# Kernel optimization log

Hardware: AMD Instinct MI355X
Metric: run time of the kernel (lower is better)

Reference implementation:

```python
import jax, jax.numpy as jnp
import numpy as np

TAU = 2.0
EPS = 1e-5
SG_ALPHA = 4.0  # spikingjelly default Sigmoid surrogate alpha


@jax.custom_vjp
def heaviside(x):
    return (x >= 0.0).astype(x.dtype)

def _heaviside_fwd(x):
    return heaviside(x), x

def _heaviside_bwd(x, g):
    s = jax.nn.sigmoid(SG_ALPHA * x)
    return (g * SG_ALPHA * s * (1.0 - s),)

heaviside.defvjp(_heaviside_fwd, _heaviside_bwd)


def lif(x_seq, v_th):
    """Multi-step LIF, hard reset to 0, detach_reset=True. x_seq: (T, ...)."""
    def step(v, x_t):
        v = v + (x_t - v) / TAU
        s = heaviside(v - v_th)
        v = v * (1.0 - jax.lax.stop_gradient(s))  # detached hard reset
        return v, s
    _, spikes = jax.lax.scan(step, jnp.zeros_like(x_seq[0]), x_seq)
    return spikes


def bn(y, gamma, beta, mean, var):
    # y: (T, B, C, N); inference-mode BatchNorm1d over channel dim
    inv = gamma / jnp.sqrt(var + EPS)
    return y * inv[None, None, :, None] + (beta - mean * inv)[None, None, :, None]


def setup_inputs() -> dict:
    key = jax.random.key(0)
    ks = jax.random.split(key, 8)
    T, B, C, H, W = 4, 32, 256, 32, 32
    d = {
        "x": jax.random.normal(ks[0], (T, B, C, H, W), jnp.float32),
        "q_w": jax.random.normal(ks[1], (C, C), jnp.float32) * (1.0 / np.sqrt(C)),
        "q_gamma": jnp.ones((C,), jnp.float32),
        "q_beta": jnp.zeros((C,), jnp.float32),
        "q_mean": jnp.zeros((C,), jnp.float32),
        "q_var": jnp.ones((C,), jnp.float32),
        "k_w": jax.random.normal(ks[2], (C, C), jnp.float32) * (1.0 / np.sqrt(C)),
        "k_gamma": jnp.ones((C,), jnp.float32),
        "k_beta": jnp.zeros((C,), jnp.float32),
        "k_mean": jnp.zeros((C,), jnp.float32),
        "k_var": jnp.ones((C,), jnp.float32),
        "p_w": jax.random.normal(ks[3], (C, C), jnp.float32) * (1.0 / np.sqrt(C)),
        "p_b": jnp.zeros((C,), jnp.float32),
        "p_gamma": jnp.ones((C,), jnp.float32),
        "p_beta": jnp.zeros((C,), jnp.float32),
        "p_mean": jnp.zeros((C,), jnp.float32),
        "p_var": jnp.ones((C,), jnp.float32),
    }
    return d


def reference(x, q_w, q_gamma, q_beta, q_mean, q_var,
              k_w, k_gamma, k_beta, k_mean, k_var,
              p_w, p_b, p_gamma, p_beta, p_mean, p_var):
    T, B, C, H, W = x.shape
    num_heads = 8
    dh = C // num_heads
    N = H * W
    xs = x.reshape(T, B, C, N)

    # Q branch: 1x1 conv (C x C matmul) -> BN -> LIF
    q = bn(jnp.einsum('oc,tbcn->tbon', q_w, xs), q_gamma, q_beta, q_mean, q_var)
    q_spikes = lif(q, 1.0)                                # (T,B,C,N)
    q_h = q_spikes.reshape(T, B, num_heads, dh, N)

    # K branch
    k = bn(jnp.einsum('oc,tbcn->tbon', k_w, xs), k_gamma, k_beta, k_mean, k_var)
    k_spikes = lif(k, 1.0)
    k_h = k_spikes.reshape(T, B, num_heads, dh, N)

    # channel-sum pooled Q per head -> attn LIF (v_th=0.5) -> elementwise mult with K
    q_sum = jnp.sum(q_h, axis=3, keepdims=True)           # (T,B,h,1,N)
    attn = lif(q_sum, 0.5)
    x_one = attn * k_h                                    # (T,B,h,dh,N)

    # projection: 1x1 conv with bias -> BN -> LIF
    xo = x_one.reshape(T, B, C, N)
    xo = jnp.einsum('oc,tbcn->tbon', p_w, xo) + p_b[None, None, :, None]
    xo = bn(xo, p_gamma, p_beta, p_mean, p_var).reshape(T, B, C, H, W)
    x_final = lif(xo, 1.0)
    return x_final
```

## Files before the change

kernel.cpp:

```cpp
#include <hip/hip_runtime.h>
#include <cstdint>
#include <cstddef>

#define T_DIM 4
#define B_DIM 32
#define C_DIM 256
#define N_DIM 1024
#define NHEAD 8
#define DHEAD 32
#define NWRD 32

__device__ __forceinline__ float lif_step(float& v, float x, float vth) {
    v = __fadd_rn(v, __fmul_rn(__fsub_rn(x, v), 0.5f));
    const float s = (v >= vth) ? 1.0f : 0.0f;
    if (s != 0.0f) v = 0.0f;
    return s;
}

__device__ __forceinline__ void async_copy16(const float* g, float* l) {
    __builtin_amdgcn_global_load_lds(
        (const __attribute__((address_space(1))) unsigned int*)g,
        (__attribute__((address_space(3))) unsigned int*)l, 16, 0, 0);
}

#define FMA_ROW(r, av)                                \
    acc[(r)*8+0] = fmaf(av, b0.x, acc[(r)*8+0]);      \
    acc[(r)*8+1] = fmaf(av, b0.y, acc[(r)*8+1]);      \
    acc[(r)*8+2] = fmaf(av, b0.z, acc[(r)*8+2]);      \
    acc[(r)*8+3] = fmaf(av, b0.w, acc[(r)*8+3]);      \
    acc[(r)*8+4] = fmaf(av, b1.x, acc[(r)*8+4]);      \
    acc[(r)*8+5] = fmaf(av, b1.y, acc[(r)*8+5]);      \
    acc[(r)*8+6] = fmaf(av, b1.z, acc[(r)*8+6]);      \
    acc[(r)*8+7] = fmaf(av, b1.w, acc[(r)*8+7]);

#define FMA_8x8()        \
    FMA_ROW(0, a0.x)     \
    FMA_ROW(1, a0.y)     \
    FMA_ROW(2, a0.z)     \
    FMA_ROW(3, a0.w)     \
    FMA_ROW(4, a1.x)     \
    FMA_ROW(5, a1.y)     \
    FMA_ROW(6, a1.z)     \
    FMA_ROW(7, a1.w)

__global__ __launch_bounds__(256) void k_transpose(
    const float* __restrict__ qw, const float* __restrict__ kw,
    const float* __restrict__ pw, float* __restrict__ wqk_t,
    float* __restrict__ p_t)
{
    const int i = blockIdx.x * 256 + threadIdx.x;
    if (i < C_DIM * 512) {
        const int k = i >> 9, col = i & 511;
        const int h = col >> 6, j = col & 63;
        wqk_t[i] = (j < 32) ? qw[(size_t)(h * 32 + j) * C_DIM + k]
                            : kw[(size_t)(h * 32 + j - 32) * C_DIM + k];
    } else {
        const int i2 = i - C_DIM * 512;
        const int k = i2 >> 8, c = i2 & 255;
        p_t[i2] = pw[(size_t)c * C_DIM + k];
    }
}

__global__ __launch_bounds__(256, 3) void k_qk(
    const float* __restrict__ x, const float* __restrict__ wqk,
    const float* __restrict__ qg, const float* __restrict__ qbeta,
    const float* __restrict__ qmean, const float* __restrict__ qvar,
    const float* __restrict__ kg, const float* __restrict__ kbeta,
    const float* __restrict__ kmean, const float* __restrict__ kvar,
    uint32_t* __restrict__ xbits)
{
    __shared__ float w_lds[32 * 128];
    __shared__ float x_lds[32 * 128];
    __shared__ float inv_lds[128];
    __shared__ float bias_lds[128];
    float*    qsum_lds = x_lds;
    float*    attn_lds = x_lds + 256;
    uint32_t* pack_lds = (uint32_t*)(x_lds + 512);

    const int tid = threadIdx.x;
    const int hp = blockIdx.x, nt = blockIdx.y, b = blockIdx.z;
    const int n0g = nt * 128;

    const int  mg   = tid >> 4;
    const int  m0   = mg << 3;
    const int  ng   = tid & 15;
    const int  n0   = ng << 2;
    const int  hsel = mg >> 3;
    const bool is_q = ((mg & 7) < 4);

    if (tid < 128) {
        const int m = tid;
        const int hs = m >> 6, j = m & 63;
        const int h = hp * 2 + hs;
        const bool q = (j < 32);
        const float* g  = q ? qg    : kg;
        const float* be = q ? qbeta : kbeta;
        const float* me = q ? qmean : kmean;
        const float* va = q ? qvar  : kvar;
        const int ch = h * DHEAD + (q ? j : j - 32);
        const float iv = __fdiv_rn(g[ch], __fsqrt_rn(__fadd_rn(va[ch], 1e-5f)));
        inv_lds[m]  = iv;
        bias_lds[m] = __fsub_rn(be[ch], __fmul_rn(me[ch], iv));
    }

    const int skl  = tid >> 5;
    const int scol = (tid & 31) << 2;
    const float* wgp = wqk + (size_t)skl * 512 + hp * 128 + scol;

    float vstate[64];
    #pragma unroll
    for (int i = 0; i < 64; i++) vstate[i] = 0.0f;
    float v_attn = 0.0f;

    for (int t = 0; t < T_DIM; ++t) {
        float acc[64];
        #pragma unroll
        for (int i = 0; i < 64; i++) acc[i] = 0.0f;

        const float* xgp = x + ((size_t)(t * B_DIM + b) * C_DIM + skl) * N_DIM
                           + n0g + scol;

        for (int c = 0; c < 8; ++c) {
            const int kk = c * 32;
            __syncthreads();
            #pragma unroll
            for (int r = 0; r < 4; r++) {
                async_copy16(wgp + (size_t)(kk + r * 8) * 512, w_lds + r * 1024 + tid * 4);
                async_copy16(xgp + (size_t)(kk + r * 8) * N_DIM, x_lds + r * 1024 + tid * 4);
            }
            __syncthreads();
            #pragma unroll 2
            for (int k = 0; k < 32; k++) {
                const float4 a0 = *(const float4*)(w_lds + k * 128 + m0);
                const float4 a1 = *(const float4*)(w_lds + k * 128 + m0 + 4);
                const float4 b0 = *(const float4*)(x_lds + k * 128 + n0);
                const float4 b1 = *(const float4*)(x_lds + k * 128 + 64 + n0);
                FMA_8x8()
            }
        }

        #pragma unroll
        for (int r = 0; r < 8; r++) {
            const float iv = inv_lds[m0 + r];
            const float bs = bias_lds[m0 + r];
            #pragma unroll
            for (int j = 0; j < 8; j++) {
                const float y = __fadd_rn(__fmul_rn(acc[r * 8 + j], iv), bs);
                acc[r * 8 + j] = lif_step(vstate[r * 8 + j], y, 1.0f);
            }
        }

        __syncthreads();
        qsum_lds[tid] = 0.0f;
        pack_lds[tid] = 0u;
        __syncthreads();

        if (is_q) {
            #pragma unroll
            for (int j = 0; j < 8; j++) {
                const int col = (j < 4) ? (n0 + j) : (64 + n0 + (j - 4));
                float cs = acc[j];
                #pragma unroll
                for (int r = 1; r < 8; r++) cs += acc[r * 8 + j];
                atomicAdd(&qsum_lds[hsel * 128 + col], cs);
            }
        }
        __syncthreads();
        attn_lds[tid] = lif_step(v_attn, qsum_lds[tid], 0.5f);
        __syncthreads();

        if (!is_q) {
            #pragma unroll
            for (int r = 0; r < 8; r++) {
                const int krow = ((mg & 7) - 4) * 8 + r;
                #pragma unroll
                for (int ci = 0; ci < 2; ci++) {
                    uint32_t nib = 0;
                    #pragma unroll
                    for (int jj = 0; jj < 4; jj++) {
                        const int col = ci * 64 + n0 + jj;
                        if (acc[r * 8 + ci * 4 + jj] != 0.0f &&
                            attn_lds[hsel * 128 + col] != 0.0f)
                            nib |= (1u << jj);
                    }
                    if (nib) {
                        const int word = ci * 2 + (ng >> 3);
                        const int shf  = (ng & 7) * 4;
                        atomicOr(&pack_lds[hsel * 128 + krow * 4 + word], nib << shf);
                    }
                }
            }
        }
        __syncthreads();
        {
            const int hs2  = tid >> 7;
            const int rem  = tid & 127;
            const int krow = rem >> 2, word = rem & 3;
            const int ch = (hp * 2 + hs2) * DHEAD + krow;
            xbits[((size_t)(t * B_DIM + b) * C_DIM + ch) * NWRD + nt * 4 + word]
                = pack_lds[tid];
        }
    }
}

__global__ __launch_bounds__(256, 3) void k_proj(
    const uint32_t* __restrict__ xbits, const float* __restrict__ pt,
    const float* __restrict__ pbias, const float* __restrict__ pg,
    const float* __restrict__ pbeta, const float* __restrict__ pmean,
    const float* __restrict__ pvar, float* __restrict__ out)
{
    __shared__ float w_lds[32 * 128];
    __shared__ float x_lds[32 * 128];
    __shared__ float inv_lds[128];
    __shared__ float bias_lds[128];
    __shared__ float pb_lds[128];

    const int tid = threadIdx.x;
    const int mt = blockIdx.x, nt = blockIdx.y, b = blockIdx.z;
    const int n0g = nt * 128;
    const int c0  = mt * 128;

    const int mg = tid >> 4, m0 = mg << 3;
    const int ng = tid & 15, n0 = ng << 2;

    if (tid < 128) {
        const int ch = c0 + tid;
        const float iv = __fdiv_rn(pg[ch], __fsqrt_rn(__fadd_rn(pvar[ch], 1e-5f)));
        inv_lds[tid]  = iv;
        bias_lds[tid] = __fsub_rn(pbeta[ch], __fmul_rn(pmean[ch], iv));
        pb_lds[tid]   = pbias[ch];
    }

    const int skl  = tid >> 5;
    const int scol = (tid & 31) << 2;
    const float* wgp = pt + (size_t)skl * 256 + c0 + scol;

    const int urow = tid >> 3, cg = tid & 7;
    const int wsel = nt * 4 + (cg >> 1);
    const int ushf = (cg & 1) * 16;
    float* xw = x_lds + tid * 16;

    float vstate[64];
    #pragma unroll
    for (int i = 0; i < 64; i++) vstate[i] = 0.0f;

    for (int t = 0; t < T_DIM; ++t) {
        float acc[64];
        #pragma unroll
        for (int i = 0; i < 64; i++) acc[i] = 0.0f;

        const uint32_t* xg = xbits + (size_t)(t * B_DIM + b) * C_DIM * NWRD;

        uint32_t u = xg[(size_t)urow * NWRD + wsel];

        for (int c = 0; c < 8; ++c) {
            __syncthreads();
            {
                const uint32_t bits = (u >> ushf) & 0xffffu;
                #pragma unroll
                for (int q4 = 0; q4 < 4; q4++) {
                    float4 f;
                    f.x = ((bits >> (q4 * 4 + 0)) & 1u) ? 1.0f : 0.0f;
                    f.y = ((bits >> (q4 * 4 + 1)) & 1u) ? 1.0f : 0.0f;
                    f.z = ((bits >> (q4 * 4 + 2)) & 1u) ? 1.0f : 0.0f;
                    f.w = ((bits >> (q4 * 4 + 3)) & 1u) ? 1.0f : 0.0f;
                    *(float4*)(xw + q4 * 4) = f;
                }
            }
            #pragma unroll
            for (int r = 0; r < 4; r++)
                async_copy16(wgp + (size_t)(c * 32 + r * 8) * 256,
                             w_lds + r * 1024 + tid * 4);
            __syncthreads();
            if (c + 1 < 8)
                u = xg[(size_t)((c + 1) * 32 + urow) * NWRD + wsel];
            #pragma unroll 2
            for (int k = 0; k < 32; k++) {
                const float4 a0 = *(const float4*)(w_lds + k * 128 + m0);
                const float4 a1 = *(const float4*)(w_lds + k * 128 + m0 + 4);
                const float4 b0 = *(const float4*)(x_lds + k * 128 + n0);
                const float4 b1 = *(const float4*)(x_lds + k * 128 + 64 + n0);
                FMA_8x8()
            }
        }

        #pragma unroll
        for (int r = 0; r < 8; r++) {
            const int ch = c0 + m0 + r;
            const float iv = inv_lds[m0 + r];
            const float bs = bias_lds[m0 + r];
            const float pb = pb_lds[m0 + r];
            float* ob = out + ((size_t)(t * B_DIM + b) * C_DIM + ch) * N_DIM + n0g;
            float oAv[4], oBv[4];
            #pragma unroll
            for (int j = 0; j < 8; j++) {
                float y = __fadd_rn(acc[r * 8 + j], pb);
                y = __fadd_rn(__fmul_rn(y, iv), bs);
                const float s = lif_step(vstate[r * 8 + j], y, 1.0f);
                if (j < 4) oAv[j] = s; else oBv[j - 4] = s;
            }
            float4 oA, oB;
            oA.x = oAv[0]; oA.y = oAv[1]; oA.z = oAv[2]; oA.w = oAv[3];
            oB.x = oBv[0]; oB.y = oBv[1]; oB.z = oBv[2]; oB.w = oBv[3];
            *(float4*)(ob + n0)      = oA;
            *(float4*)(ob + 64 + n0) = oB;
        }
    }
}

extern "C" void kernel_launch(void* const* d_in, const int* in_sizes, int n_in,
                              void* d_out, int out_size, void* d_ws, size_t ws_size,
                              hipStream_t stream) {
    const float* x    = (const float*)d_in[0];
    const float* q_w  = (const float*)d_in[1];
    const float* q_g  = (const float*)d_in[2];
    const float* q_b  = (const float*)d_in[3];
    const float* q_m  = (const float*)d_in[4];
    const float* q_v  = (const float*)d_in[5];
    const float* k_w  = (const float*)d_in[6];
    const float* k_g  = (const float*)d_in[7];
    const float* k_b  = (const float*)d_in[8];
    const float* k_m  = (const float*)d_in[9];
    const float* k_v  = (const float*)d_in[10];
    const float* p_w  = (const float*)d_in[11];
    const float* p_b  = (const float*)d_in[12];
    const float* p_g  = (const float*)d_in[13];
    const float* p_be = (const float*)d_in[14];
    const float* p_m  = (const float*)d_in[15];
    const float* p_v  = (const float*)d_in[16];

    float*    wqk_t = (float*)d_ws;
    float*    p_t   = (float*)((char*)d_ws + 524288);
    uint32_t* xbits = (uint32_t*)((char*)d_ws + 786432);
    float*    out   = (float*)d_out;

    k_transpose<<<768, 256, 0, stream>>>(q_w, k_w, p_w, wqk_t, p_t);

    dim3 g1(NHEAD / 2, N_DIM / 128, B_DIM);
    k_qk<<<g1, 256, 0, stream>>>(x, wqk_t, q_g, q_b, q_m, q_v,
                                 k_g, k_b, k_m, k_v, xbits);

    dim3 g2(C_DIM / 128, N_DIM / 128, B_DIM);
    k_proj<<<g2, 256, 0, stream>>>(xbits, p_t, p_b, p_g, p_be, p_m, p_v, out);
}
```

Baseline: 829.0 us.

## Double-buffer LDS tiles in qk and proj kernels, flattening time and K loops

Both GEMM kernels now keep two LDS buffers and issue async global-to-LDS copies for the next K-chunk while the current one is being multiplied. The time and K-chunk loops are merged into a single 32-step loop, so prefetching also crosses timestep boundaries, leaving one barrier per step. The goal is to hide global load latency behind FMA work. The cost is twice the LDS footprint and launch bounds lowered from 3 to 2 blocks per CU, which cuts occupancy.

```diff
diff --git a/kernel.cpp b/kernel.cpp
--- a/kernel.cpp
+++ b/kernel.cpp
@@ -61,7 +61,7 @@
     }
 }
 
-__global__ __launch_bounds__(256, 3) void k_qk(
+__global__ __launch_bounds__(256, 2) void k_qk(
     const float* __restrict__ x, const float* __restrict__ wqk,
     const float* __restrict__ qg, const float* __restrict__ qbeta,
     const float* __restrict__ qmean, const float* __restrict__ qvar,
@@ -69,13 +69,13 @@
     const float* __restrict__ kmean, const float* __restrict__ kvar,
     uint32_t* __restrict__ xbits)
 {
-    __shared__ float w_lds[32 * 128];
-    __shared__ float x_lds[32 * 128];
+    __shared__ float w_lds[2][32 * 128];
+    __shared__ float x_lds[2][32 * 128];
     __shared__ float inv_lds[128];
     __shared__ float bias_lds[128];
-    float*    qsum_lds = x_lds;
-    float*    attn_lds = x_lds + 256;
-    uint32_t* pack_lds = (uint32_t*)(x_lds + 512);
+    __shared__ float    qsum_lds[256];
+    __shared__ float    attn_lds[256];
+    __shared__ uint32_t pack_lds[256];
 
     const int tid = threadIdx.x;
     const int hp = blockIdx.x, nt = blockIdx.y, b = blockIdx.z;
@@ -112,105 +112,120 @@
     for (int i = 0; i < 64; i++) vstate[i] = 0.0f;
     float v_attn = 0.0f;
 
-    for (int t = 0; t < T_DIM; ++t) {
-        float acc[64];
+    {
+        const float* xgp = x + ((size_t)b * C_DIM + skl) * N_DIM + n0g + scol;
         #pragma unroll
-        for (int i = 0; i < 64; i++) acc[i] = 0.0f;
-
-        const float* xgp = x + ((size_t)(t * B_DIM + b) * C_DIM + skl) * N_DIM
-                           + n0g + scol;
-
-        for (int c = 0; c < 8; ++c) {
-            const int kk = c * 32;
-            __syncthreads();
+        for (int r = 0; r < 4; r++) {
+            async_copy16(wgp + (size_t)(r * 8) * 512,  &w_lds[0][r * 1024 + tid * 4]);
+            async_copy16(xgp + (size_t)(r * 8) * N_DIM, &x_lds[0][r * 1024 + tid * 4]);
+        }
+    }
+
+    float acc[64];
+    #pragma unroll
+    for (int i = 0; i < 64; i++) acc[i] = 0.0f;
+
+    for (int g = 0; g < 32; ++g) {
+        const int cur = g & 1;
+        __syncthreads();
+        if (g + 1 < 32) {
+            const int g1 = g + 1, tt = g1 >> 3, kk = (g1 & 7) * 32;
+            const float* xgp = x + ((size_t)(tt * B_DIM + b) * C_DIM + kk + skl) * N_DIM
+                               + n0g + scol;
+            float* wd = &w_lds[1 - cur][0];
+            float* xd = &x_lds[1 - cur][0];
             #pragma unroll
             for (int r = 0; r < 4; r++) {
-                async_copy16(wgp + (size_t)(kk + r * 8) * 512, w_lds + r * 1024 + tid * 4);
-                async_copy16(xgp + (size_t)(kk + r * 8) * N_DIM, x_lds + r * 1024 + tid * 4);
-            }
-            __syncthreads();
+                async_copy16(wgp + (size_t)(kk + r * 8) * 512,  wd + r * 1024 + tid * 4);
+                async_copy16(xgp + (size_t)(r * 8) * N_DIM,     xd + r * 1024 + tid * 4);
+            }
+        }
+        {
+            const float* wl = &w_lds[cur][0];
+            const float* xl = &x_lds[cur][0];
             #pragma unroll 2
             for (int k = 0; k < 32; k++) {
-                const float4 a0 = *(const float4*)(w_lds + k * 128 + m0);
-                const float4 a1 = *(const float4*)(w_lds + k * 128 + m0 + 4);
-                const float4 b0 = *(const float4*)(x_lds + k * 128 + n0);
-                const float4 b1 = *(const float4*)(x_lds + k * 128 + 64 + n0);
+                const float4 a0 = *(const float4*)(wl + k * 128 + m0);
+                const float4 a1 = *(const float4*)(wl + k * 128 + m0 + 4);
+                const float4 b0 = *(const float4*)(xl + k * 128 + n0);
+                const float4 b1 = *(const float4*)(xl + k * 128 + 64 + n0);
                 FMA_8x8()
             }
         }
 
-        #pragma unroll
-        for (int r = 0; r < 8; r++) {
-            const float iv = inv_lds[m0 + r];
-            const float bs = bias_lds[m0 + r];
-            #pragma unroll
-            for (int j = 0; j < 8; j++) {
-                const float y = __fadd_rn(__fmul_rn(acc[r * 8 + j], iv), bs);
-                acc[r * 8 + j] = lif_step(vstate[r * 8 + j], y, 1.0f);
-            }
-        }
-
-        __syncthreads();
-        qsum_lds[tid] = 0.0f;
-        pack_lds[tid] = 0u;
-        __syncthreads();
-
-        if (is_q) {
-            #pragma unroll
-            for (int j = 0; j < 8; j++) {
-                const int col = (j < 4) ? (n0 + j) : (64 + n0 + (j - 4));
-                float cs = acc[j];
+        if ((g & 7) == 7) {
+            const int t = g >> 3;
+            #pragma unroll
+            for (int r = 0; r < 8; r++) {
+                const float iv = inv_lds[m0 + r];
+                const float bs = bias_lds[m0 + r];
                 #pragma unroll
-                for (int r = 1; r < 8; r++) cs += acc[r * 8 + j];
-                atomicAdd(&qsum_lds[hsel * 128 + col], cs);
-            }
-        }
-        __syncthreads();
-        attn_lds[tid] = lif_step(v_attn, qsum_lds[tid], 0.5f);
-        __syncthreads();
-
-        if (!is_q) {
-            #pragma unroll
-            for (int r = 0; r < 8; r++) {
-                const int krow = ((mg & 7) - 4) * 8 + r;
+                for (int j = 0; j < 8; j++) {
+                    const float y = __fadd_rn(__fmul_rn(acc[r * 8 + j], iv), bs);
+                    acc[r * 8 + j] = lif_step(vstate[r * 8 + j], y, 1.0f);
+                }
+            }
+            qsum_lds[tid] = 0.0f;
+            pack_lds[tid] = 0u;
+            __syncthreads();
+            if (is_q) {
                 #pragma unroll
-                for (int ci = 0; ci < 2; ci++) {
-                    uint32_t nib = 0;
+                for (int j = 0; j < 8; j++) {
+                    const int col = (j < 4) ? (n0 + j) : (64 + n0 + (j - 4));
+                    float cs = acc[j];
                     #pragma unroll
-                    for (int jj = 0; jj < 4; jj++) {
-                        const int col = ci * 64 + n0 + jj;
-                        if (acc[r * 8 + ci * 4 + jj] != 0.0f &&
-                            attn_lds[hsel * 128 + col] != 0.0f)
-                            nib |= (1u << jj);
-                    }
-                    if (nib) {
-                        const int word = ci * 2 + (ng >> 3);
-                        const int shf  = (ng & 7) * 4;
-                        atomicOr(&pack_lds[hsel * 128 + krow * 4 + word], nib << shf);
+                    for (int r = 1; r < 8; r++) cs += acc[r * 8 + j];
+                    atomicAdd(&qsum_lds[hsel * 128 + col], cs);
+                }
+            }
+            __syncthreads();
+            attn_lds[tid] = lif_step(v_attn, qsum_lds[tid], 0.5f);
+            __syncthreads();
+            if (!is_q) {
+                #pragma unroll
+                for (int r = 0; r < 8; r++) {
+                    const int krow = ((mg & 7) - 4) * 8 + r;
+                    #pragma unroll
+                    for (int ci = 0; ci < 2; ci++) {
+                        uint32_t nib = 0;
+                        #pragma unroll
+                        for (int jj = 0; jj < 4; jj++) {
+                            const int col = ci * 64 + n0 + jj;
+                            if (acc[r * 8 + ci * 4 + jj] != 0.0f &&
+                                attn_lds[hsel * 128 + col] != 0.0f)
+                                nib |= (1u << jj);
+                        }
+                        if (nib) {
+                            const int word = ci * 2 + (ng >> 3);
+                            const int shf  = (ng & 7) * 4;
+                            atomicOr(&pack_lds[hsel * 128 + krow * 4 + word], nib << shf);
+                        }
                     }
                 }
             }
-        }
-        __syncthreads();
-        {
-            const int hs2  = tid >> 7;
-            const int rem  = tid & 127;
-            const int krow = rem >> 2, word = rem & 3;
-            const int ch = (hp * 2 + hs2) * DHEAD + krow;
-            xbits[((size_t)(t * B_DIM + b) * C_DIM + ch) * NWRD + nt * 4 + word]
-                = pack_lds[tid];
-        }
-    }
-}
-
-__global__ __launch_bounds__(256, 3) void k_proj(
+            __syncthreads();
+            {
+                const int hs2  = tid >> 7;
+                const int rem  = tid & 127;
+                const int krow = rem >> 2, word = rem & 3;
+                const int ch = (hp * 2 + hs2) * DHEAD + krow;
+                xbits[((size_t)(t * B_DIM + b) * C_DIM + ch) * NWRD + nt * 4 + word]
+                    = pack_lds[tid];
+            }
+            #pragma unroll
+            for (int i = 0; i < 64; i++) acc[i] = 0.0f;
+        }
+    }
+}
+
+__global__ __launch_bounds__(256, 2) void k_proj(
     const uint32_t* __restrict__ xbits, const float* __restrict__ pt,
     const float* __restrict__ pbias, const float* __restrict__ pg,
     const float* __restrict__ pbeta, const float* __restrict__ pmean,
     const float* __restrict__ pvar, float* __restrict__ out)
 {
-    __shared__ float w_lds[32 * 128];
-    __shared__ float x_lds[32 * 128];
+    __shared__ float w_lds[2][32 * 128];
+    __shared__ float x_lds[2][32 * 128];
     __shared__ float inv_lds[128];
     __shared__ float bias_lds[128];
     __shared__ float pb_lds[128];
@@ -238,74 +253,100 @@
     const int urow = tid >> 3, cg = tid & 7;
     const int wsel = nt * 4 + (cg >> 1);
     const int ushf = (cg & 1) * 16;
-    float* xw = x_lds + tid * 16;
 
     float vstate[64];
     #pragma unroll
     for (int i = 0; i < 64; i++) vstate[i] = 0.0f;
 
-    for (int t = 0; t < T_DIM; ++t) {
-        float acc[64];
+    #define BITS_AT(G) xbits[((size_t)((G) >> 3) * B_DIM + b) * C_DIM * NWRD \
+                             + (size_t)(((G) & 7) * 32 + urow) * NWRD + wsel]
+
+    {
+        const uint32_t u0 = BITS_AT(0);
+        const uint32_t bits = (u0 >> ushf) & 0xffffu;
+        float* xw = &x_lds[0][tid * 16];
         #pragma unroll
-        for (int i = 0; i < 64; i++) acc[i] = 0.0f;
-
-        const uint32_t* xg = xbits + (size_t)(t * B_DIM + b) * C_DIM * NWRD;
-
-        uint32_t u = xg[(size_t)urow * NWRD + wsel];
-
-        for (int c = 0; c < 8; ++c) {
-            __syncthreads();
-            {
-                const uint32_t bits = (u >> ushf) & 0xffffu;
-                #pragma unroll
-                for (int q4 = 0; q4 < 4; q4++) {
-                    float4 f;
-                    f.x = ((bits >> (q4 * 4 + 0)) & 1u) ? 1.0f : 0.0f;
-                    f.y = ((bits >> (q4 * 4 + 1)) & 1u) ? 1.0f : 0.0f;
-                    f.z = ((bits >> (q4 * 4 + 2)) & 1u) ? 1.0f : 0.0f;
-                    f.w = ((bits >> (q4 * 4 + 3)) & 1u) ? 1.0f : 0.0f;
-                    *(float4*)(xw + q4 * 4) = f;
-                }
-            }
+        for (int q4 = 0; q4 < 4; q4++) {
+            float4 f;
+            f.x = ((bits >> (q4 * 4 + 0)) & 1u) ? 1.0f : 0.0f;
+            f.y = ((bits >> (q4 * 4 + 1)) & 1u) ? 1.0f : 0.0f;
+            f.z = ((bits >> (q4 * 4 + 2)) & 1u) ? 1.0f : 0.0f;
+            f.w = ((bits >> (q4 * 4 + 3)) & 1u) ? 1.0f : 0.0f;
+            *(float4*)(xw + q4 * 4) = f;
+        }
+        #pragma unroll
+        for (int r = 0; r < 4; r++)
+            async_copy16(wgp + (size_t)(r * 8) * 256, &w_lds[0][r * 1024 + tid * 4]);
+    }
+    uint32_t u_a = BITS_AT(1);
+
+    float acc[64];
+    #pragma unroll
+    for (int i = 0; i < 64; i++) acc[i] = 0.0f;
+
+    for (int g = 0; g < 32; ++g) {
+        const int cur = g & 1;
+        __syncthreads();
+        if (g + 1 < 32) {
+            const int kk = ((g + 1) & 7) * 32;
+            const uint32_t bits = (u_a >> ushf) & 0xffffu;
+            float* xw = &x_lds[1 - cur][tid * 16];
+            #pragma unroll
+            for (int q4 = 0; q4 < 4; q4++) {
+                float4 f;
+                f.x = ((bits >> (q4 * 4 + 0)) & 1u) ? 1.0f : 0.0f;
+                f.y = ((bits >> (q4 * 4 + 1)) & 1u) ? 1.0f : 0.0f;
+                f.z = ((bits >> (q4 * 4 + 2)) & 1u) ? 1.0f : 0.0f;
+                f.w = ((bits >> (q4 * 4 + 3)) & 1u) ? 1.0f : 0.0f;
+                *(float4*)(xw + q4 * 4) = f;
+            }
+            float* wd = &w_lds[1 - cur][0];
             #pragma unroll
             for (int r = 0; r < 4; r++)
-                async_copy16(wgp + (size_t)(c * 32 + r * 8) * 256,
-                             w_lds + r * 1024 + tid * 4);
-            __syncthreads();
-            if (c + 1 < 8)
-                u = xg[(size_t)((c + 1) * 32 + urow) * NWRD + wsel];
+                async_copy16(wgp + (size_t)(kk + r * 8) * 256, wd + r * 1024 + tid * 4);
+        }
+        if (g + 2 < 32) u_a = BITS_AT(g + 2);
+        {
+            const float* wl = &w_lds[cur][0];
+            const float* xl = &x_lds[cur][0];
             #pragma unroll 2
             for (int k = 0; k < 32; k++) {
-                const float4 a0 = *(const float4*)(w_lds + k * 128 + m0);
-                const float4 a1 = *(const float4*)(w_lds + k * 128 + m0 + 4);
-                const float4 b0 = *(const float4*)(x_lds + k * 128 + n0);
-                const float4 b1 = *(const float4*)(x_lds + k * 128 + 64 + n0);
+                const float4 a0 = *(const float4*)(wl + k * 128 + m0);
+                const float4 a1 = *(const float4*)(wl + k * 128 + m0 + 4);
+                const float4 b0 = *(const float4*)(xl + k * 128 + n0);
+                const float4 b1 = *(const float4*)(xl + k * 128 + 64 + n0);
                 FMA_8x8()
             }
         }
 
-        #pragma unroll
-        for (int r = 0; r < 8; r++) {
-            const int ch = c0 + m0 + r;
-            const float iv = inv_lds[m0 + r];
-            const float bs = bias_lds[m0 + r];
-            const float pb = pb_lds[m0 + r];
-            float* ob = out + ((size_t)(t * B_DIM + b) * C_DIM + ch) * N_DIM + n0g;
-            float oAv[4], oBv[4];
-            #pragma unroll
-            for (int j = 0; j < 8; j++) {
-                float y = __fadd_rn(acc[r * 8 + j], pb);
-                y = __fadd_rn(__fmul_rn(y, iv), bs);
-                const float s = lif_step(vstate[r * 8 + j], y, 1.0f);
-                if (j < 4) oAv[j] = s; else oBv[j - 4] = s;
-            }
-            float4 oA, oB;
-            oA.x = oAv[0]; oA.y = oAv[1]; oA.z = oAv[2]; oA.w = oAv[3];
-            oB.x = oBv[0]; oB.y = oBv[1]; oB.z = oBv[2]; oB.w = oBv[3];
-            *(float4*)(ob + n0)      = oA;
-            *(float4*)(ob + 64 + n0) = oB;
-        }
-    }
+        if ((g & 7) == 7) {
+            const int t = g >> 3;
+            #pragma unroll
+            for (int r = 0; r < 8; r++) {
+                const int ch = c0 + m0 + r;
+                const float iv = inv_lds[m0 + r];
+                const float bs = bias_lds[m0 + r];
+                const float pb = pb_lds[m0 + r];
+                float* ob = out + ((size_t)(t * B_DIM + b) * C_DIM + ch) * N_DIM + n0g;
+                float oAv[4], oBv[4];
+                #pragma unroll
+                for (int j = 0; j < 8; j++) {
+                    float y = __fadd_rn(acc[r * 8 + j], pb);
+                    y = __fadd_rn(__fmul_rn(y, iv), bs);
+                    const float s = lif_step(vstate[r * 8 + j], y, 1.0f);
+                    if (j < 4) oAv[j] = s; else oBv[j - 4] = s;
+                }
+                float4 oA, oB;
+                oA.x = oAv[0]; oA.y = oAv[1]; oA.z = oAv[2]; oA.w = oAv[3];
+                oB.x = oBv[0]; oB.y = oBv[1]; oB.z = oBv[2]; oB.w = oBv[3];
+                *(float4*)(ob + n0)      = oA;
+                *(float4*)(ob + 64 + n0) = oB;
+            }
+            #pragma unroll
+            for (int i = 0; i < 64; i++) acc[i] = 0.0f;
+        }
+    }
+    #undef BITS_AT
 }
 
 extern "C" void kernel_launch(void* const* d_in, const int* in_sizes, int n_in,
```

After: 825.9 us. Within noise of the previous version (-0.4%).
